# Performance work log

Measured on AMD Instinct MI355X. Metric: run time of the kernel, lower is better.

The kernel has to match this reference:

```python
import jax, jax.numpy as jnp
import numpy as np

U, I, D, L, NNZ = 8000, 16000, 64, 2, 768000
N = U + I


def setup_inputs() -> dict:
    key = jax.random.key(0)
    ks = jax.random.split(key, 10)
    return {
        "user_indices": jnp.arange(U, dtype=jnp.int64) if jax.config.jax_enable_x64 else jnp.arange(U, dtype=jnp.int32),
        "item_indices": jnp.arange(I, dtype=jnp.int32),
        "adj_rows": jax.random.randint(ks[0], (NNZ,), 0, N, dtype=jnp.int32),
        "adj_cols": jax.random.randint(ks[1], (NNZ,), 0, N, dtype=jnp.int32),
        "adj_vals": jax.random.uniform(ks[2], (NNZ,), dtype=jnp.float32),
        "user_emb": 0.1 * jax.random.normal(ks[3], (U, D), dtype=jnp.float32),
        "item_emb": 0.1 * jax.random.normal(ks[4], (I, D), dtype=jnp.float32),
        "gc_W": 0.05 * jax.random.normal(ks[5], (L, D, D), dtype=jnp.float32),
        "gc_b": jnp.zeros((L, D), dtype=jnp.float32),
        "bi_W": 0.05 * jax.random.normal(ks[6], (L, D, D), dtype=jnp.float32),
        "bi_b": jnp.zeros((L, D), dtype=jnp.float32),
    }


def reference(user_indices, item_indices, adj_rows, adj_cols, adj_vals,
              user_emb, item_emb, gc_W, gc_b, bi_W, bi_b):
    # embedding lookups + concat -> ego embeddings [N, D]
    ego = jnp.concatenate([user_emb[user_indices], item_emb[item_indices]], axis=0)
    n_nodes = ego.shape[0]
    all_embeddings = [ego]
    n_layers = gc_W.shape[0]
    for l in range(n_layers):
        # sparse.mm(adj, ego): gather neighbor rows, weight, scatter-add to rows
        side = jax.ops.segment_sum(adj_vals[:, None] * ego[adj_cols], adj_rows,
                                   num_segments=n_nodes)  # [N, D]
        sum_emb = jax.nn.leaky_relu(side @ gc_W[l].T + gc_b[l], negative_slope=0.01)
        bi_emb = jax.nn.leaky_relu((ego * side) @ bi_W[l].T + bi_b[l], negative_slope=0.01)
        ego = sum_emb + bi_emb
        all_embeddings.append(ego)
    all_emb = jnp.concatenate(all_embeddings, axis=1)  # [N, D*(L+1)]
    n_users = user_indices.shape[0]
    u_g = all_emb[:n_users]
    i_g = all_emb[n_users:]
    scores = u_g @ i_g.T  # [U, I]
    return jax.nn.log_softmax(scores, axis=1)
```

## Files before the change

### kernel.cpp

```cpp
#include <hip/hip_runtime.h>
#include <hip/hip_bf16.h>
#include <math.h>

#define NU   8000
#define NI   16000
#define NN   24000
#define DD   64
#define NL   2
#define NNZS 768000
#define KD   192
#define NCH  25
#define ACHUNK 640
#define CTILES 5
#define RBLK3 42
#define CBLK 125
#define SCH  24

typedef __attribute__((ext_vector_type(8))) short  short8;
typedef __attribute__((ext_vector_type(4))) float  f32x4;

__device__ __forceinline__ unsigned short f2bf(float x) {
    union { float f; unsigned int u; } v; v.f = x;
    unsigned int r = v.u + 0x7fff + ((v.u >> 16) & 1);
    return (unsigned short)(r >> 16);
}
__device__ __forceinline__ float bf2f(unsigned short u) {
    union { unsigned int u; float f; } v; v.u = ((unsigned int)u) << 16;
    return v.f;
}

__device__ __forceinline__ int bslot(int nf, int kt, int g, int r16) {
    return ((((kt * 8 + nf) * 4 + g) * 16) + r16) ^ ((g + 4 * kt) & 7);
}

__global__ void k_concat(const int* __restrict__ uidx, const int* __restrict__ iidx,
                         const float* __restrict__ ue, const float* __restrict__ ie,
                         const float* __restrict__ gcW, const float* __restrict__ biW,
                         unsigned short* __restrict__ allemb,
                         unsigned short* __restrict__ wbf, int* __restrict__ cnt) {
    int t = blockIdx.x * blockDim.x + threadIdx.x;
    if (t < NN) cnt[t] = 0;
    if (t < NL * DD * DD) {
        wbf[t] = f2bf(gcW[t]);
        wbf[NL * DD * DD + t] = f2bf(biW[t]);
    }
    if (t >= NN * DD) return;
    int n = t >> 6, d = t & 63;
    float v = (n < NU) ? ue[uidx[n] * DD + d] : ie[iidx[n - NU] * DD + d];
    allemb[(size_t)n * KD + d] = f2bf(v);
}

__global__ void k_hist(const int* __restrict__ rows, int* __restrict__ cnt) {
    int e = blockIdx.x * blockDim.x + threadIdx.x;
    if (e < NNZS) atomicAdd(&cnt[rows[e]], 1);
}

__global__ __launch_bounds__(1024) void k_scan1(const int* __restrict__ cnt,
                                                int* __restrict__ rp, int* __restrict__ btot) {
    __shared__ int wsum[16];
    int tid = threadIdx.x, lane = tid & 63, wid = tid >> 6;
    int i = blockIdx.x * 1024 + tid;
    int v = (i < NN) ? cnt[i] : 0;
    int x = v;
#pragma unroll
    for (int off = 1; off < 64; off <<= 1) {
        int t = __shfl_up(x, off, 64);
        if (lane >= off) x += t;
    }
    if (lane == 63) wsum[wid] = x;
    __syncthreads();
    if (tid < 16) {
        int y = wsum[tid];
#pragma unroll
        for (int off = 1; off < 16; off <<= 1) {
            int t = __shfl_up(y, off, 64);
            if (tid >= off) y += t;
        }
        wsum[tid] = y;
    }
    __syncthreads();
    int incl = x + (wid ? wsum[wid - 1] : 0);
    if (i < NN) rp[i + 1] = incl;
    if (tid == 0) btot[blockIdx.x] = wsum[15];
}

__global__ void k_scan2(const int* __restrict__ btot, int* __restrict__ boff) {
    int tid = threadIdx.x;
    int v = (tid < SCH) ? btot[tid] : 0;
    int x = v;
#pragma unroll
    for (int off = 1; off < 32; off <<= 1) {
        int t = __shfl_up(x, off, 64);
        if (tid >= off) x += t;
    }
    if (tid < SCH) boff[tid] = x - v;
}

__global__ __launch_bounds__(1024) void k_scan3(const int* __restrict__ cnt,
                                                const int* __restrict__ boff,
                                                int* __restrict__ rp, int* __restrict__ wp) {
    int i = blockIdx.x * 1024 + threadIdx.x;
    if (i == 0) rp[0] = 0;
    if (i >= NN) return;
    int g = rp[i + 1] + boff[blockIdx.x];
    rp[i + 1] = g;
    wp[i] = g - cnt[i];
}

__global__ void k_scatter(const int* __restrict__ rows, const int* __restrict__ cols,
                          const float* __restrict__ vals, int* __restrict__ wp,
                          int2* __restrict__ edat) {
    int e = blockIdx.x * blockDim.x + threadIdx.x;
    if (e >= NNZS) return;
    int r = rows[e];
    int pos = atomicAdd(&wp[r], 1);
    edat[pos] = make_int2(cols[e], __float_as_int(vals[e]));
}

__global__ void k_spmm_csr(const int* __restrict__ rp, const int2* __restrict__ edat,
                           const unsigned short* __restrict__ feat, float* __restrict__ side) {
    int lane = threadIdx.x & 63;
    int wave = (blockIdx.x * blockDim.x + threadIdx.x) >> 6;
    int nw   = (gridDim.x * blockDim.x) >> 6;
    for (int r = wave; r < NN; r += nw) {
        int e0 = rp[r], e1 = rp[r + 1];
        float acc = 0.f;
        int e = e0;
        for (; e + 8 <= e1; e += 8) {
            int2 d[8];
#pragma unroll
            for (int j = 0; j < 8; ++j) d[j] = edat[e + j];
#pragma unroll
            for (int j = 0; j < 8; ++j)
                acc = fmaf(__int_as_float(d[j].y), bf2f(feat[(size_t)d[j].x * KD + lane]), acc);
        }
        for (; e < e1; ++e) {
            int2 d = edat[e];
            acc = fmaf(__int_as_float(d.y), bf2f(feat[(size_t)d.x * KD + lane]), acc);
        }
        side[(size_t)r * DD + lane] = acc;
    }
}

__global__ __launch_bounds__(256) void k_dense(const float* __restrict__ side,
                        unsigned short* __restrict__ allemb, int l,
                        const unsigned short* __restrict__ wg_bf,
                        const unsigned short* __restrict__ wb_bf,
                        const float* __restrict__ gcb, const float* __restrict__ bib) {
    int lane = threadIdx.x & 63;
    int wave = threadIdx.x >> 6;
    int n0 = (blockIdx.x * 4 + wave) * 16;
    int nrow = lane & 15;
    int kofs = (lane >> 4) * 8;
    const unsigned short* feat = allemb + l * DD;

    short8 bg[4][2], bb[4][2];
#pragma unroll
    for (int nf = 0; nf < 4; ++nf)
#pragma unroll
        for (int kt = 0; kt < 2; ++kt) {
            bg[nf][kt] = *(const short8*)(wg_bf + (nf * 16 + nrow) * DD + kt * 32 + kofs);
            bb[nf][kt] = *(const short8*)(wb_bf + (nf * 16 + nrow) * DD + kt * 32 + kofs);
        }

    short8 a1[2], a2[2];
    const float* sp = side + (size_t)(n0 + nrow) * DD;
    const unsigned short* ep = feat + (size_t)(n0 + nrow) * KD;
#pragma unroll
    for (int kt = 0; kt < 2; ++kt) {
        int o = kt * 32 + kofs;
#pragma unroll
        for (int j = 0; j < 8; ++j) {
            float s = sp[o + j];
            float e = bf2f(ep[o + j]);
            a1[kt][j] = (short)f2bf(s);
            a2[kt][j] = (short)f2bf(e * s);
        }
    }

    f32x4 acc1[4], acc2[4];
#pragma unroll
    for (int nf = 0; nf < 4; ++nf) { acc1[nf] = (f32x4){0,0,0,0}; acc2[nf] = (f32x4){0,0,0,0}; }
#pragma unroll
    for (int nf = 0; nf < 4; ++nf)
#pragma unroll
        for (int kt = 0; kt < 2; ++kt) {
            acc1[nf] = __builtin_amdgcn_mfma_f32_16x16x32_bf16(a1[kt], bg[nf][kt], acc1[nf], 0, 0, 0);
            acc2[nf] = __builtin_amdgcn_mfma_f32_16x16x32_bf16(a2[kt], bb[nf][kt], acc2[nf], 0, 0, 0);
        }

    int g = lane >> 4;
#pragma unroll
    for (int nf = 0; nf < 4; ++nf) {
        int o = nf * 16 + nrow;
        float b1 = gcb[o], b2 = bib[o];
#pragma unroll
        for (int r = 0; r < 4; ++r) {
            int node = n0 + g * 4 + r;
            float v1 = acc1[nf][r] + b1;
            float v2 = acc2[nf][r] + b2;
            v1 = v1 > 0.f ? v1 : 0.01f * v1;
            v2 = v2 > 0.f ? v2 : 0.01f * v2;
            allemb[(size_t)node * KD + (l + 1) * DD + o] = f2bf(v1 + v2);
        }
    }
}

__global__ __launch_bounds__(256) void k_lse_part(const unsigned short* __restrict__ allemb,
                                                  float* __restrict__ pm, float* __restrict__ ps) {
    __shared__ short8 Bs[3072];
    int id = blockIdx.x;
    int rowblk = id % RBLK3;
    int chunk  = id / RBLK3;
    int tid = threadIdx.x;
    int lane = tid & 63;
    int wave = tid >> 6;
    int r0 = rowblk * 192 + wave * 48;
    int c0 = chunk * ACHUNK;
    const unsigned short* A = allemb;
    const unsigned short* B = allemb + (size_t)NU * KD;
    int kofs = (lane >> 4) * 8;
    int g = lane >> 4;

    short8 a[3][6];
#pragma unroll
    for (int mi = 0; mi < 3; ++mi) {
        int ar = r0 + mi * 16 + (lane & 15);
        if (ar >= NU) ar = NU - 1;
#pragma unroll
        for (int kt = 0; kt < 6; ++kt)
            a[mi][kt] = *(const short8*)(A + (size_t)ar * KD + kt * 32 + kofs);
    }

    float m[3][4], s[3][4];
#pragma unroll
    for (int mi = 0; mi < 3; ++mi)
#pragma unroll
        for (int r = 0; r < 4; ++r) { m[mi][r] = -INFINITY; s[mi][r] = 0.f; }

    for (int t = 0; t < CTILES; ++t) {
        const unsigned short* Bt = B + (size_t)(c0 + t * 128) * KD;
        __syncthreads();
#pragma unroll
        for (int i = 0; i < 12; ++i) {
            int mm = i * 256 + tid;
            int r = mm / 24, c = mm - r * 24;
            int kt = c >> 2, gg = c & 3;
            Bs[bslot(r >> 4, kt, gg, r & 15)] = *(const short8*)(Bt + (size_t)r * KD + c * 8);
        }
        __syncthreads();

        f32x4 acc[3][8];
#pragma unroll
        for (int mi = 0; mi < 3; ++mi)
#pragma unroll
            for (int nf = 0; nf < 8; ++nf) acc[mi][nf] = (f32x4){0.f, 0.f, 0.f, 0.f};
#pragma unroll
        for (int nf = 0; nf < 8; ++nf)
#pragma unroll
            for (int kt = 0; kt < 6; ++kt) {
                short8 b = Bs[bslot(nf, kt, g, lane & 15)];
#pragma unroll
                for (int mi = 0; mi < 3; ++mi)
                    acc[mi][nf] = __builtin_amdgcn_mfma_f32_16x16x32_bf16(a[mi][kt], b, acc[mi][nf], 0, 0, 0);
            }
#pragma unroll
        for (int mi = 0; mi < 3; ++mi)
#pragma unroll
            for (int r = 0; r < 4; ++r) {
                float lm = acc[mi][0][r];
#pragma unroll
                for (int nf = 1; nf < 8; ++nf) lm = fmaxf(lm, acc[mi][nf][r]);
                float nm = fmaxf(m[mi][r], lm);
                float p = 0.f;
#pragma unroll
                for (int nf = 0; nf < 8; ++nf) p += __expf(acc[mi][nf][r] - nm);
                s[mi][r] = s[mi][r] * __expf(m[mi][r] - nm) + p;
                m[mi][r] = nm;
            }
    }
#pragma unroll
    for (int mi = 0; mi < 3; ++mi)
#pragma unroll
        for (int r = 0; r < 4; ++r) {
            float mm = m[mi][r], ss = s[mi][r];
#pragma unroll
            for (int off = 1; off < 16; off <<= 1) {
                float om = __shfl_xor(mm, off, 64);
                float os = __shfl_xor(ss, off, 64);
                float nm = fmaxf(mm, om);
                ss = ss * __expf(mm - nm) + os * __expf(om - nm);
                mm = nm;
            }
            m[mi][r] = mm; s[mi][r] = ss;
        }
    if ((lane & 15) == 0) {
#pragma unroll
        for (int mi = 0; mi < 3; ++mi)
#pragma unroll
            for (int r = 0; r < 4; ++r) {
                int row = r0 + mi * 16 + g * 4 + r;
                if (row < NU) {
                    pm[chunk * NU + row] = m[mi][r];
                    ps[chunk * NU + row] = s[mi][r];
                }
            }
    }
}

__global__ void k_lse_comb(const float* __restrict__ pm, const float* __restrict__ ps,
                           float* __restrict__ lse) {
    int r = blockIdx.x * blockDim.x + threadIdx.x;
    if (r >= NU) return;
    float m = -INFINITY;
    for (int c = 0; c < NCH; ++c) m = fmaxf(m, pm[c * NU + r]);
    float s = 0.f;
    for (int c = 0; c < NCH; ++c) s += ps[c * NU + r] * __expf(pm[c * NU + r] - m);
    lse[r] = m + __logf(s);
}

__global__ __launch_bounds__(256) void k_out(const unsigned short* __restrict__ allemb,
                                             const float* __restrict__ lse, float* __restrict__ out) {
    __shared__ short8 Bs[3072];
    int id = blockIdx.x;
    int rowblk = id / CBLK;
    int colblk = id % CBLK;
    int tid = threadIdx.x;
    int lane = tid & 63;
    int wave = tid >> 6;
    int r0 = rowblk * 192 + wave * 48;
    int c0 = colblk * 128;
    const unsigned short* A = allemb;
    const unsigned short* B = allemb + (size_t)NU * KD;
    int kofs = (lane >> 4) * 8;
    int g = lane >> 4;

    const unsigned short* Bt = B + (size_t)c0 * KD;
#pragma unroll
    for (int i = 0; i < 12; ++i) {
        int mm = i * 256 + tid;
        int r = mm / 24, c = mm - r * 24;
        int kt = c >> 2, gg = c & 3;
        Bs[bslot(r >> 4, kt, gg, r & 15)] = *(const short8*)(Bt + (size_t)r * KD + c * 8);
    }

    short8 a[3][6];
#pragma unroll
    for (int mi = 0; mi < 3; ++mi) {
        int ar = r0 + mi * 16 + (lane & 15);
        if (ar >= NU) ar = NU - 1;
#pragma unroll
        for (int kt = 0; kt < 6; ++kt)
            a[mi][kt] = *(const short8*)(A + (size_t)ar * KD + kt * 32 + kofs);
    }
    float l4[3][4];
#pragma unroll
    for (int mi = 0; mi < 3; ++mi)
#pragma unroll
        for (int r = 0; r < 4; ++r) {
            int row = r0 + mi * 16 + g * 4 + r;
            l4[mi][r] = lse[row >= NU ? NU - 1 : row];
        }
    __syncthreads();

    f32x4 acc[3][8];
#pragma unroll
    for (int mi = 0; mi < 3; ++mi)
#pragma unroll
        for (int nf = 0; nf < 8; ++nf) acc[mi][nf] = (f32x4){0.f, 0.f, 0.f, 0.f};
#pragma unroll
    for (int nf = 0; nf < 8; ++nf)
#pragma unroll
        for (int kt = 0; kt < 6; ++kt) {
            short8 b = Bs[bslot(nf, kt, g, lane & 15)];
#pragma unroll
            for (int mi = 0; mi < 3; ++mi)
                acc[mi][nf] = __builtin_amdgcn_mfma_f32_16x16x32_bf16(a[mi][kt], b, acc[mi][nf], 0, 0, 0);
        }
    __syncthreads();

    float* tilef = (float*)Bs;
    float* tW = tilef + wave * 16 * 132;
#pragma unroll
    for (int mi = 0; mi < 3; ++mi) {
        int rowbase = r0 + mi * 16;
#pragma unroll
        for (int nf = 0; nf < 8; ++nf)
#pragma unroll
            for (int r = 0; r < 4; ++r)
                tW[(g * 4 + r) * 132 + nf * 16 + (lane & 15)] = acc[mi][nf][r] - l4[mi][r];
#pragma unroll
        for (int it = 0; it < 8; ++it) {
            int idx = it * 64 + lane;
            int rr = idx >> 5;
            int cc = (idx & 31) * 4;
            int row = rowbase + rr;
            if (row < NU) {
                f32x4 v = *(const f32x4*)&tW[rr * 132 + cc];
                __builtin_nontemporal_store(v, (f32x4*)&out[(size_t)row * NI + c0 + cc]);
            }
        }
    }
}

extern "C" void kernel_launch(void* const* d_in, const int* in_sizes, int n_in,
                              void* d_out, int out_size, void* d_ws, size_t ws_size,
                              hipStream_t stream) {
    const int*   uidx = (const int*)d_in[0];
    const int*   iidx = (const int*)d_in[1];
    const int*   arow = (const int*)d_in[2];
    const int*   acol = (const int*)d_in[3];
    const float* aval = (const float*)d_in[4];
    const float* ue   = (const float*)d_in[5];
    const float* ie   = (const float*)d_in[6];
    const float* gcW  = (const float*)d_in[7];
    const float* gcb  = (const float*)d_in[8];
    const float* biW  = (const float*)d_in[9];
    const float* bib  = (const float*)d_in[10];
    float* out = (float*)d_out;

    char* w = (char*)d_ws;
    unsigned short* allemb = (unsigned short*)w;  w += (size_t)NN * KD * sizeof(unsigned short);
    float* side = (float*)w;                      w += (size_t)NN * DD * sizeof(float);
    float* pm  = (float*)w;                       w += (size_t)NCH * NU * sizeof(float);
    float* ps  = (float*)w;                       w += (size_t)NCH * NU * sizeof(float);
    float* lse = (float*)w;                       w += (size_t)NU * sizeof(float);
    unsigned short* wbf = (unsigned short*)w;     w += (size_t)2 * NL * DD * DD * sizeof(unsigned short);
    int* cnt   = (int*)w;                         w += (size_t)NN * sizeof(int);
    int* rp    = (int*)w;                         w += (size_t)(NN + 4) * sizeof(int);
    int* wp    = (int*)w;                         w += (size_t)NN * sizeof(int);
    int* btot  = (int*)w;                         w += 32 * sizeof(int);
    int* boff  = (int*)w;                         w += 32 * sizeof(int);
    int2* edat = (int2*)w;                        w += (size_t)NNZS * sizeof(int2);

    unsigned short* wg_bf = wbf;
    unsigned short* wb_bf = wbf + NL * DD * DD;

    k_concat<<<(NN * DD + 255) / 256, 256, 0, stream>>>(uidx, iidx, ue, ie, gcW, biW,
                                                        allemb, wbf, cnt);

    k_hist<<<(NNZS + 255) / 256, 256, 0, stream>>>(arow, cnt);
    k_scan1<<<SCH, 1024, 0, stream>>>(cnt, rp, btot);
    k_scan2<<<1, 64, 0, stream>>>(btot, boff);
    k_scan3<<<SCH, 1024, 0, stream>>>(cnt, boff, rp, wp);
    k_scatter<<<(NNZS + 255) / 256, 256, 0, stream>>>(arow, acol, aval, wp, edat);

    for (int l = 0; l < NL; ++l) {
        k_spmm_csr<<<3000, 256, 0, stream>>>(rp, edat, allemb + l * DD, side);
        k_dense<<<NN / 64, 256, 0, stream>>>(side, allemb, l,
                                             wg_bf + l * DD * DD, wb_bf + l * DD * DD,
                                             gcb + l * DD, bib + l * DD);
    }

    k_lse_part<<<RBLK3 * NCH, 256, 0, stream>>>(allemb, pm, ps);
    k_lse_comb<<<(NU + 255) / 256, 256, 0, stream>>>(pm, ps, lse);
    k_out<<<RBLK3 * CBLK, 256, 0, stream>>>(allemb, lse, out);
}
```

Before: 453.5 us.

## Fuse three-pass scan into single-block scan; split SpMM wave into two edge halves

Replaces the three-kernel prefix scan (block scan, block-total scan, fixup) with a single 1024-thread block where each thread serially scans 24 counts, removing two kernel launches and the intermediate buffers. The SpMM kernel now has each half-wave handle alternate edges, with every lane loading two packed bf16 features as one 32-bit load, and combines the halves with a cross-half shuffle. This doubles the number of edges in flight per row and halves the load instructions, at the cost of an extra reduction step. The single-block scan reads strided (non-coalesced) and runs on only one CU.

```diff
diff --git a/kernel.cpp b/kernel.cpp
--- a/kernel.cpp
+++ b/kernel.cpp
@@ -14,7 +14,6 @@
 #define CTILES 5
 #define RBLK3 42
 #define CBLK 125
-#define SCH  24
 
 typedef __attribute__((ext_vector_type(8))) short  short8;
 typedef __attribute__((ext_vector_type(4))) float  f32x4;
@@ -55,13 +54,21 @@
     if (e < NNZS) atomicAdd(&cnt[rows[e]], 1);
 }
 
-__global__ __launch_bounds__(1024) void k_scan1(const int* __restrict__ cnt,
-                                                int* __restrict__ rp, int* __restrict__ btot) {
+__global__ __launch_bounds__(1024) void k_scan(const int* __restrict__ cnt,
+                                               int* __restrict__ rp, int* __restrict__ wp) {
     __shared__ int wsum[16];
+    const int PT = 24;
     int tid = threadIdx.x, lane = tid & 63, wid = tid >> 6;
-    int i = blockIdx.x * 1024 + tid;
-    int v = (i < NN) ? cnt[i] : 0;
-    int x = v;
+    int base = tid * PT;
+    int v[PT];
+    int sum = 0;
+#pragma unroll
+    for (int j = 0; j < PT; ++j) {
+        int i = base + j;
+        v[j] = (i < NN) ? cnt[i] : 0;
+        sum += v[j];
+    }
+    int x = sum;
 #pragma unroll
     for (int off = 1; off < 64; off <<= 1) {
         int t = __shfl_up(x, off, 64);
@@ -79,32 +86,17 @@
         wsum[tid] = y;
     }
     __syncthreads();
-    int incl = x + (wid ? wsum[wid - 1] : 0);
-    if (i < NN) rp[i + 1] = incl;
-    if (tid == 0) btot[blockIdx.x] = wsum[15];
-}
-
-__global__ void k_scan2(const int* __restrict__ btot, int* __restrict__ boff) {
-    int tid = threadIdx.x;
-    int v = (tid < SCH) ? btot[tid] : 0;
-    int x = v;
-#pragma unroll
-    for (int off = 1; off < 32; off <<= 1) {
-        int t = __shfl_up(x, off, 64);
-        if (tid >= off) x += t;
-    }
-    if (tid < SCH) boff[tid] = x - v;
-}
-
-__global__ __launch_bounds__(1024) void k_scan3(const int* __restrict__ cnt,
-                                                const int* __restrict__ boff,
-                                                int* __restrict__ rp, int* __restrict__ wp) {
-    int i = blockIdx.x * 1024 + threadIdx.x;
-    if (i == 0) rp[0] = 0;
-    if (i >= NN) return;
-    int g = rp[i + 1] + boff[blockIdx.x];
-    rp[i + 1] = g;
-    wp[i] = g - cnt[i];
+    int run = (x - sum) + (wid ? wsum[wid - 1] : 0);
+    if (tid == 0) rp[0] = 0;
+#pragma unroll
+    for (int j = 0; j < PT; ++j) {
+        int i = base + j;
+        if (i < NN) {
+            run += v[j];
+            rp[i + 1] = run;
+            wp[i] = run - v[j];
+        }
+    }
 }
 
 __global__ void k_scatter(const int* __restrict__ rows, const int* __restrict__ cols,
@@ -120,25 +112,45 @@
 __global__ void k_spmm_csr(const int* __restrict__ rp, const int2* __restrict__ edat,
                            const unsigned short* __restrict__ feat, float* __restrict__ side) {
     int lane = threadIdx.x & 63;
+    int half = lane >> 5;
+    int hl   = lane & 31;
     int wave = (blockIdx.x * blockDim.x + threadIdx.x) >> 6;
     int nw   = (gridDim.x * blockDim.x) >> 6;
     for (int r = wave; r < NN; r += nw) {
         int e0 = rp[r], e1 = rp[r + 1];
-        float acc = 0.f;
-        int e = e0;
-        for (; e + 8 <= e1; e += 8) {
-            int2 d[8];
-#pragma unroll
-            for (int j = 0; j < 8; ++j) d[j] = edat[e + j];
-#pragma unroll
-            for (int j = 0; j < 8; ++j)
-                acc = fmaf(__int_as_float(d[j].y), bf2f(feat[(size_t)d[j].x * KD + lane]), acc);
-        }
-        for (; e < e1; ++e) {
+        float ax = 0.f, ay = 0.f;
+        int e = e0 + half;
+        for (; e + 6 < e1; e += 8) {
+            int2 d0 = edat[e],     d1 = edat[e + 2];
+            int2 d2 = edat[e + 4], d3 = edat[e + 6];
+            unsigned int p0 = *(const unsigned int*)(feat + (size_t)d0.x * KD + hl * 2);
+            unsigned int p1 = *(const unsigned int*)(feat + (size_t)d1.x * KD + hl * 2);
+            unsigned int p2 = *(const unsigned int*)(feat + (size_t)d2.x * KD + hl * 2);
+            unsigned int p3 = *(const unsigned int*)(feat + (size_t)d3.x * KD + hl * 2);
+            float v0 = __int_as_float(d0.y), v1 = __int_as_float(d1.y);
+            float v2 = __int_as_float(d2.y), v3 = __int_as_float(d3.y);
+            ax = fmaf(v0, bf2f((unsigned short)(p0 & 0xffff)), ax);
+            ay = fmaf(v0, bf2f((unsigned short)(p0 >> 16)), ay);
+            ax = fmaf(v1, bf2f((unsigned short)(p1 & 0xffff)), ax);
+            ay = fmaf(v1, bf2f((unsigned short)(p1 >> 16)), ay);
+            ax = fmaf(v2, bf2f((unsigned short)(p2 & 0xffff)), ax);
+            ay = fmaf(v2, bf2f((unsigned short)(p2 >> 16)), ay);
+            ax = fmaf(v3, bf2f((unsigned short)(p3 & 0xffff)), ax);
+            ay = fmaf(v3, bf2f((unsigned short)(p3 >> 16)), ay);
+        }
+        for (; e < e1; e += 2) {
             int2 d = edat[e];
-            acc = fmaf(__int_as_float(d.y), bf2f(feat[(size_t)d.x * KD + lane]), acc);
-        }
-        side[(size_t)r * DD + lane] = acc;
+            unsigned int p = *(const unsigned int*)(feat + (size_t)d.x * KD + hl * 2);
+            float v = __int_as_float(d.y);
+            ax = fmaf(v, bf2f((unsigned short)(p & 0xffff)), ax);
+            ay = fmaf(v, bf2f((unsigned short)(p >> 16)), ay);
+        }
+        ax += __shfl_xor(ax, 32, 64);
+        ay += __shfl_xor(ay, 32, 64);
+        if (half == 0) {
+            float2 o = make_float2(ax, ay);
+            *(float2*)&side[(size_t)r * DD + hl * 2] = o;
+        }
     }
 }
 
@@ -429,8 +441,6 @@
     int* cnt   = (int*)w;                         w += (size_t)NN * sizeof(int);
     int* rp    = (int*)w;                         w += (size_t)(NN + 4) * sizeof(int);
     int* wp    = (int*)w;                         w += (size_t)NN * sizeof(int);
-    int* btot  = (int*)w;                         w += 32 * sizeof(int);
-    int* boff  = (int*)w;                         w += 32 * sizeof(int);
     int2* edat = (int2*)w;                        w += (size_t)NNZS * sizeof(int2);
 
     unsigned short* wg_bf = wbf;
@@ -440,9 +450,7 @@
                                                         allemb, wbf, cnt);
 
     k_hist<<<(NNZS + 255) / 256, 256, 0, stream>>>(arow, cnt);
-    k_scan1<<<SCH, 1024, 0, stream>>>(cnt, rp, btot);
-    k_scan2<<<1, 64, 0, stream>>>(btot, boff);
-    k_scan3<<<SCH, 1024, 0, stream>>>(cnt, boff, rp, wp);
+    k_scan<<<1, 1024, 0, stream>>>(cnt, rp, wp);
     k_scatter<<<(NNZS + 255) / 256, 256, 0, stream>>>(arow, acol, aval, wp, edat);
 
     for (int l = 0; l < NL; ++l) {
```

After: 470.5 us, median of 2. +3.8%, slower.
